# Performance work log

Hardware: AMD Instinct MI355X
Metric: run time of the kernel (lower is better)

The kernel has to match this reference:

```python
import jax, jax.numpy as jnp
import numpy as np
import math

PS = 8  # patch size (hard-coded in module)
DEPTH = 6
LAMBDA_INIT = 0.8 - 0.6 * math.exp(-0.3 * DEPTH)

# torch_dct norm=None DCT-II matrix: y_k = 2 * sum_n x_n cos(pi*(2n+1)k/(2N))
_n = np.arange(PS)
_C = 2.0 * np.cos(np.pi * (2 * _n[None, :] + 1) * _n[:, None] / (2 * PS))  # [k, n]
_Ci = np.linalg.inv(_C)
DCT_M = jnp.asarray(_C, jnp.float32)
IDCT_M = jnp.asarray(_Ci, jnp.float32)


def dct2(x):  # 2D DCT over last two dims (torch_dct.dct_2d, norm=None)
    return jnp.einsum('...mn,am,bn->...ab', x, DCT_M, DCT_M)


def idct2(x):  # exact inverse (torch_dct.idct_2d, norm=None)
    return jnp.einsum('...ab,ma,nb->...mn', x, IDCT_M, IDCT_M)


def conv1x1(x, w):  # w: [O, I]
    return jnp.einsum('oi,bihw->bohw', w, x)


def dw3(x, w):  # depthwise 3x3, stride 1, pad 1; w: [C, 1, 3, 3]
    return jax.lax.conv_general_dilated(
        x, w, window_strides=(1, 1), padding='SAME',
        dimension_numbers=('NCHW', 'OIHW', 'NCHW'),
        feature_group_count=x.shape[1])


def prelu(t, a):
    return jnp.where(t >= 0, t, a * t)


def setup_inputs() -> dict:
    key = jax.random.key(0)
    ks = jax.random.split(key, 20)
    b, c, H, W = 2, 64, 384, 384
    w = lambda k, shape: jax.random.normal(k, shape, jnp.float32) * 0.05
    heads = c // 16
    return {
        'x': jax.random.normal(ks[0], (b, c, H, W), jnp.float32),
        'nir': jax.random.normal(ks[1], (b, c, H, W), jnp.float32),
        'w_hidden': w(ks[2], (c, c)),
        'w_hidden_nir': w(ks[3], (2 * c, c)),
        'w_dw': w(ks[4], (c, 1, 3, 3)),
        'w_dw_nir': w(ks[5], (2 * c, 1, 3, 3)),
        'temperature': jnp.ones((heads, 1, 1), jnp.float32),
        'w_proj_mid': w(ks[6], (c, c)),
        'w_proj_out': w(ks[7], (c, c)),
        'w_p1a': w(ks[8], (c, 1, 3, 3)),
        'a_p1': jnp.asarray(0.25, jnp.float32),
        'w_p1b': w(ks[9], (c, 1, 3, 3)),
        'w_p2a': w(ks[10], (c, 1, 3, 3)),
        'a_p2': jnp.asarray(0.25, jnp.float32),
        'w_p2b': w(ks[11], (c, 1, 3, 3)),
        'lq1': jax.random.normal(ks[12], (c,), jnp.float32) * 0.1,
        'lk1': jax.random.normal(ks[13], (c,), jnp.float32) * 0.1,
        'lq2': jax.random.normal(ks[14], (c,), jnp.float32) * 0.1,
        'lk2': jax.random.normal(ks[15], (c,), jnp.float32) * 0.1,
    }


def reference(x, nir, w_hidden, w_hidden_nir, w_dw, w_dw_nir, temperature,
              w_proj_mid, w_proj_out, w_p1a, a_p1, w_p1b, w_p2a, a_p2, w_p2b,
              lq1, lk1, lq2, lk2):
    b, c, H, W = x.shape
    heads = c // 16
    hh, ww = H // PS, W // PS

    hidden = conv1x1(x, w_hidden)
    nir_hidden = conv1x1(nir, w_hidden_nir)
    q = dw3(hidden, w_dw)
    kv = dw3(nir_hidden, w_dw_nir)
    k, v = kv[:, :c], kv[:, c:]

    # b c (hh p1) (ww p2) -> b c hh ww p1 p2
    patch = lambda t: t.reshape(b, c, hh, PS, ww, PS).transpose(0, 1, 2, 4, 3, 5)
    q_fft = dct2(patch(q))
    k_fft = dct2(patch(k))
    out1 = q_fft * k_fft

    L = hh * ww * PS * PS
    hf = lambda t: t.reshape(b, heads, c // heads, L)  # b head c L
    q_fft, k_fft, out1f = hf(q_fft), hf(k_fft), hf(out1)

    qn = q_fft / jnp.maximum(jnp.linalg.norm(q_fft, axis=-1, keepdims=True), 1e-12)
    kn = k_fft / jnp.maximum(jnp.linalg.norm(k_fft, axis=-1, keepdims=True), 1e-12)

    attn = jax.nn.softmax(jnp.einsum('bhcl,bhdl->bhcd', qn, kn) * temperature, axis=-1)
    o = jnp.einsum('bhcd,bhdl->bhcl', attn, out1f)

    o = o.reshape(b, c, hh, ww, PS, PS)
    o = idct2(o)
    o = o.transpose(0, 1, 2, 4, 3, 5).reshape(b, c, H, W)
    out = conv1x1(o, w_proj_mid)

    lam1 = jnp.exp(jnp.sum(lq1 * lk1))
    lam2 = jnp.exp(jnp.sum(lq2 * lk2))
    lam = lam1 - lam2 + LAMBDA_INIT

    pool = lambda t, wa, a, wb: dw3(prelu(dw3(t, wa), a), wb)
    output = pool(q * out, w_p1a, a_p1, w_p1b) + pool(v - lam * (v * out), w_p2a, a_p2, w_p2b)
    return conv1x1(output, w_proj_out)
```

## Files before the change

kernel.cpp:

```cpp
#include <hip/hip_runtime.h>
#include <cmath>

#ifndef M_PI
#define M_PI 3.14159265358979323846
#endif

#define NB      2
#define N_PIX   147456
#define L_LEN   147456
#define TENS_SZ ((long)NB * 64 * N_PIX)

#define OFF_C    0
#define OFF_CI   64
#define OFF_LAM  128
#define OFF_GRAM 256
#define OFF_QQ   2304
#define OFF_KK   2432
#define OFF_ATTN 2560

#define TW 128
#define TH 16
#define LW 136
#define LH 18
#define PLH 20

__global__ __launch_bounds__(64) void init_k(const float* __restrict__ lq1, const float* __restrict__ lk1,
                                             const float* __restrict__ lq2, const float* __restrict__ lk2,
                                             float* __restrict__ sm) {
  int t = threadIdx.x;
  int a = t >> 3, m = t & 7;
  double cv = 2.0 * cos(M_PI * (double)((2 * m + 1) * a) / 16.0);
  sm[OFF_C + a * 8 + m] = (float)cv;
  sm[OFF_CI + m * 8 + a] = (float)(cv / ((a == 0) ? 32.0 : 16.0));
  float p1 = lq1[t] * lk1[t];
  float p2 = lq2[t] * lk2[t];
  #pragma unroll
  for (int off = 32; off; off >>= 1) {
    p1 += __shfl_xor(p1, off, 64);
    p2 += __shfl_xor(p2, off, 64);
  }
  if (t == 0) sm[OFF_LAM] = expf(p1) - expf(p2) + 0.70082066706704813f;
  for (int i = t; i < 2304; i += 64) sm[OFF_GRAM + i] = 0.f;
}

__global__ void diag_k(float* out, float v) { out[0] = v; }

__global__ __launch_bounds__(256) void conv1x1_k(const float* __restrict__ in, const float* __restrict__ w,
                                                 float* __restrict__ out) {
  __shared__ float ws[4096];
  int t = threadIdx.x;
  for (int j = t; j < 1024; j += 256)
    *reinterpret_cast<float4*>(ws + j * 4) = *reinterpret_cast<const float4*>(w + j * 4);
  __syncthreads();

  long gp = (long)blockIdx.x * 256;
  int bb = (int)(gp / N_PIX);
  int p0 = (int)(gp - (long)bb * N_PIX);
  int lane = t & 63;
  int co0 = (t >> 6) * 16;

  const float* ip = in + (long)bb * 64 * N_PIX + p0 + lane * 4;
  const float* wp = ws + co0 * 64;

  float acc[16][4];
  #pragma unroll
  for (int j = 0; j < 16; j++)
    #pragma unroll
    for (int p = 0; p < 4; p++) acc[j][p] = 0.f;

  for (int c4 = 0; c4 < 16; c4++) {
    float4 x0 = *reinterpret_cast<const float4*>(ip + (long)(c4 * 4 + 0) * N_PIX);
    float4 x1 = *reinterpret_cast<const float4*>(ip + (long)(c4 * 4 + 1) * N_PIX);
    float4 x2 = *reinterpret_cast<const float4*>(ip + (long)(c4 * 4 + 2) * N_PIX);
    float4 x3 = *reinterpret_cast<const float4*>(ip + (long)(c4 * 4 + 3) * N_PIX);
    #pragma unroll
    for (int j = 0; j < 16; j++) {
      float4 w4 = *reinterpret_cast<const float4*>(wp + j * 64 + c4 * 4);
      acc[j][0] = fmaf(w4.x, x0.x, acc[j][0]);
      acc[j][0] = fmaf(w4.y, x1.x, acc[j][0]);
      acc[j][0] = fmaf(w4.z, x2.x, acc[j][0]);
      acc[j][0] = fmaf(w4.w, x3.x, acc[j][0]);
      acc[j][1] = fmaf(w4.x, x0.y, acc[j][1]);
      acc[j][1] = fmaf(w4.y, x1.y, acc[j][1]);
      acc[j][1] = fmaf(w4.z, x2.y, acc[j][1]);
      acc[j][1] = fmaf(w4.w, x3.y, acc[j][1]);
      acc[j][2] = fmaf(w4.x, x0.z, acc[j][2]);
      acc[j][2] = fmaf(w4.y, x1.z, acc[j][2]);
      acc[j][2] = fmaf(w4.z, x2.z, acc[j][2]);
      acc[j][2] = fmaf(w4.w, x3.z, acc[j][2]);
      acc[j][3] = fmaf(w4.x, x0.w, acc[j][3]);
      acc[j][3] = fmaf(w4.y, x1.w, acc[j][3]);
      acc[j][3] = fmaf(w4.z, x2.w, acc[j][3]);
      acc[j][3] = fmaf(w4.w, x3.w, acc[j][3]);
    }
  }

  float* op = out + (long)bb * 64 * N_PIX + p0 + lane * 4;
  #pragma unroll
  for (int j = 0; j < 16; j++)
    *reinterpret_cast<float4*>(op + (long)(co0 + j) * N_PIX) =
        make_float4(acc[j][0], acc[j][1], acc[j][2], acc[j][3]);
}

__global__ __launch_bounds__(256) void conv1x1_nir2_k(const float* __restrict__ in, const float* __restrict__ w,
                                                      float* __restrict__ outk, float* __restrict__ outv) {
  __shared__ float ws[4096];
  int t = threadIdx.x;
  long gp = (long)blockIdx.x * 256;
  int bb = (int)(gp / N_PIX);
  int p0 = (int)(gp - (long)bb * N_PIX);
  int lane = t & 63;
  int co0 = (t >> 6) * 16;
  const float* ip = in + (long)bb * 64 * N_PIX + p0 + lane * 4;

  for (int half = 0; half < 2; half++) {
    __syncthreads();
    for (int j = t; j < 1024; j += 256)
      *reinterpret_cast<float4*>(ws + j * 4) = *reinterpret_cast<const float4*>(w + half * 4096 + j * 4);
    __syncthreads();
    const float* wp = ws + co0 * 64;
    float acc[16][4];
    #pragma unroll
    for (int j = 0; j < 16; j++)
      #pragma unroll
      for (int p = 0; p < 4; p++) acc[j][p] = 0.f;
    for (int c4 = 0; c4 < 16; c4++) {
      float4 x0 = *reinterpret_cast<const float4*>(ip + (long)(c4 * 4 + 0) * N_PIX);
      float4 x1 = *reinterpret_cast<const float4*>(ip + (long)(c4 * 4 + 1) * N_PIX);
      float4 x2 = *reinterpret_cast<const float4*>(ip + (long)(c4 * 4 + 2) * N_PIX);
      float4 x3 = *reinterpret_cast<const float4*>(ip + (long)(c4 * 4 + 3) * N_PIX);
      #pragma unroll
      for (int j = 0; j < 16; j++) {
        float4 w4 = *reinterpret_cast<const float4*>(wp + j * 64 + c4 * 4);
        acc[j][0] = fmaf(w4.x, x0.x, acc[j][0]);
        acc[j][0] = fmaf(w4.y, x1.x, acc[j][0]);
        acc[j][0] = fmaf(w4.z, x2.x, acc[j][0]);
        acc[j][0] = fmaf(w4.w, x3.x, acc[j][0]);
        acc[j][1] = fmaf(w4.x, x0.y, acc[j][1]);
        acc[j][1] = fmaf(w4.y, x1.y, acc[j][1]);
        acc[j][1] = fmaf(w4.z, x2.y, acc[j][1]);
        acc[j][1] = fmaf(w4.w, x3.y, acc[j][1]);
        acc[j][2] = fmaf(w4.x, x0.z, acc[j][2]);
        acc[j][2] = fmaf(w4.y, x1.z, acc[j][2]);
        acc[j][2] = fmaf(w4.z, x2.z, acc[j][2]);
        acc[j][2] = fmaf(w4.w, x3.z, acc[j][2]);
        acc[j][3] = fmaf(w4.x, x0.w, acc[j][3]);
        acc[j][3] = fmaf(w4.y, x1.w, acc[j][3]);
        acc[j][3] = fmaf(w4.z, x2.w, acc[j][3]);
        acc[j][3] = fmaf(w4.w, x3.w, acc[j][3]);
      }
    }
    float* op = (half ? outv : outk) + (long)bb * 64 * N_PIX + p0 + lane * 4;
    #pragma unroll
    for (int j = 0; j < 16; j++)
      *reinterpret_cast<float4*>(op + (long)(co0 + j) * N_PIX) =
          make_float4(acc[j][0], acc[j][1], acc[j][2], acc[j][3]);
  }
}

__device__ __forceinline__ float4 load_g4(const float* __restrict__ p, int gy, int gx) {
  if ((unsigned)gy >= 384u) return make_float4(0.f, 0.f, 0.f, 0.f);
  if (gx >= 0 && gx + 3 < 384) return *reinterpret_cast<const float4*>(p + gy * 384 + gx);
  float e[4];
  #pragma unroll
  for (int i = 0; i < 4; i++) {
    int xx = gx + i;
    e[i] = ((unsigned)xx < 384u) ? p[gy * 384 + xx] : 0.f;
  }
  return make_float4(e[0], e[1], e[2], e[3]);
}

__global__ __launch_bounds__(256) void dw3t_k(const float* __restrict__ in, const float* __restrict__ w,
                                              float* __restrict__ out) {
  __shared__ float sT[LH * LW];
  int plane = blockIdx.z;
  int ch = plane & 63;
  int x0 = blockIdx.x * TW, y0 = blockIdx.y * TH;
  const float* ip = in + (long)plane * N_PIX;
  int t = threadIdx.x;
  for (int j = t; j < LH * 34; j += 256) {
    int row = j / 34, c4 = j - row * 34;
    *reinterpret_cast<float4*>(sT + row * LW + c4 * 4) = load_g4(ip, y0 - 1 + row, x0 - 4 + c4 * 4);
  }
  __syncthreads();
  const float* wp = w + ch * 9;
  float w00 = wp[0], w01 = wp[1], w02 = wp[2];
  float w10 = wp[3], w11 = wp[4], w12 = wp[5];
  float w20 = wp[6], w21 = wp[7], w22 = wp[8];
  int col = t & 127, rg = t >> 7;
  int lc = col + 4;
  int r0 = rg * 8;
  float a0 = sT[r0 * LW + lc - 1],       a1 = sT[r0 * LW + lc],       a2 = sT[r0 * LW + lc + 1];
  float b0 = sT[(r0 + 1) * LW + lc - 1], b1 = sT[(r0 + 1) * LW + lc], b2 = sT[(r0 + 1) * LW + lc + 1];
  float* op = out + (long)plane * N_PIX + (long)(y0 + rg * 8) * 384 + x0 + col;
  #pragma unroll
  for (int i = 0; i < 8; i++) {
    int lr = r0 + i + 2;
    float c0 = sT[lr * LW + lc - 1], c1 = sT[lr * LW + lc], c2 = sT[lr * LW + lc + 1];
    float s = w00 * a0;
    s = fmaf(w01, a1, s); s = fmaf(w02, a2, s);
    s = fmaf(w10, b0, s); s = fmaf(w11, b1, s); s = fmaf(w12, b2, s);
    s = fmaf(w20, c0, s); s = fmaf(w21, c1, s); s = fmaf(w22, c2, s);
    op[i * 384] = s;
    a0 = b0; a1 = b1; a2 = b2;
    b0 = c0; b1 = c1; b2 = c2;
  }
}

__global__ __launch_bounds__(256) void dw3dct_k(const float* __restrict__ in, const float* __restrict__ w,
                                                const float* __restrict__ sm,
                                                float* __restrict__ outf, float* __restrict__ outs) {
  __shared__ float sT[LH * LW];
  __shared__ float Cm[64];
  int t = threadIdx.x;
  if (t < 64) Cm[t] = sm[OFF_C + t];
  int plane = blockIdx.z;
  int ch = plane & 63;
  int x0 = blockIdx.x * TW, y0 = blockIdx.y * TH;
  const float* ip = in + (long)plane * N_PIX;
  for (int j = t; j < LH * 34; j += 256) {
    int row = j / 34, c4 = j - row * 34;
    *reinterpret_cast<float4*>(sT + row * LW + c4 * 4) = load_g4(ip, y0 - 1 + row, x0 - 4 + c4 * 4);
  }
  __syncthreads();
  const float* wp = w + ch * 9;
  float w00 = wp[0], w01 = wp[1], w02 = wp[2];
  float w10 = wp[3], w11 = wp[4], w12 = wp[5];
  float w20 = wp[6], w21 = wp[7], w22 = wp[8];
  int col = t & 127, rg = t >> 7;
  int lc = col + 4;
  int r0 = rg * 8;
  float r[8];
  {
    float a0 = sT[r0 * LW + lc - 1],       a1 = sT[r0 * LW + lc],       a2 = sT[r0 * LW + lc + 1];
    float b0 = sT[(r0 + 1) * LW + lc - 1], b1 = sT[(r0 + 1) * LW + lc], b2 = sT[(r0 + 1) * LW + lc + 1];
    #pragma unroll
    for (int i = 0; i < 8; i++) {
      int lr = r0 + i + 2;
      float c0 = sT[lr * LW + lc - 1], c1 = sT[lr * LW + lc], c2 = sT[lr * LW + lc + 1];
      float s = w00 * a0;
      s = fmaf(w01, a1, s); s = fmaf(w02, a2, s);
      s = fmaf(w10, b0, s); s = fmaf(w11, b1, s); s = fmaf(w12, b2, s);
      s = fmaf(w20, c0, s); s = fmaf(w21, c1, s); s = fmaf(w22, c2, s);
      r[i] = s;
      a0 = b0; a1 = b1; a2 = b2;
      b0 = c0; b1 = c1; b2 = c2;
    }
  }
  if (outs) {
    float* op = outs + (long)plane * N_PIX + (long)(y0 + r0) * 384 + x0 + col;
    #pragma unroll
    for (int i = 0; i < 8; i++) op[i * 384] = r[i];
  }
  __syncthreads();
  #pragma unroll
  for (int i = 0; i < 8; i++) sT[(r0 + i + 1) * LW + lc] = r[i];
  __syncthreads();
  int patch = t >> 3, a = t & 7;
  int prow = patch >> 4, pcol = patch & 15;
  const float* xb = sT + (prow * 8 + 1) * LW + pcol * 8 + 4;
  float T[8];
  #pragma unroll
  for (int n = 0; n < 8; n++) {
    float s = 0.f;
    #pragma unroll
    for (int m = 0; m < 8; m++) s = fmaf(Cm[a * 8 + m], xb[m * LW + n], s);
    T[n] = s;
  }
  float o[8];
  #pragma unroll
  for (int b8 = 0; b8 < 8; b8++) {
    float s = 0.f;
    #pragma unroll
    for (int n = 0; n < 8; n++) s = fmaf(Cm[b8 * 8 + n], T[n], s);
    o[b8] = s;
  }
  int py = (y0 >> 3) + prow, px = (x0 >> 3) + pcol;
  float* op = outf + (long)plane * L_LEN + (long)(py * 48 + px) * 64 + a * 8;
  *reinterpret_cast<float4*>(op)     = make_float4(o[0], o[1], o[2], o[3]);
  *reinterpret_cast<float4*>(op + 4) = make_float4(o[4], o[5], o[6], o[7]);
}

__device__ __forceinline__ void stencil_col9(const float* __restrict__ sb, int ci, int rs0,
                                             float w00, float w01, float w02,
                                             float w10, float w11, float w12,
                                             float w20, float w21, float w22,
                                             float alpha, bool xok, int y0,
                                             float* __restrict__ r) {
  float a0 = sb[rs0 * LW + ci - 1],       a1 = sb[rs0 * LW + ci],       a2 = sb[rs0 * LW + ci + 1];
  float b0 = sb[(rs0 + 1) * LW + ci - 1], b1 = sb[(rs0 + 1) * LW + ci], b2 = sb[(rs0 + 1) * LW + ci + 1];
  #pragma unroll
  for (int ii = 0; ii < 9; ii++) {
    int rs2 = rs0 + ii + 2;
    float c0 = sb[rs2 * LW + ci - 1], c1 = sb[rs2 * LW + ci], c2 = sb[rs2 * LW + ci + 1];
    float s = w00 * a0;
    s = fmaf(w01, a1, s); s = fmaf(w02, a2, s);
    s = fmaf(w10, b0, s); s = fmaf(w11, b1, s); s = fmaf(w12, b2, s);
    s = fmaf(w20, c0, s); s = fmaf(w21, c1, s); s = fmaf(w22, c2, s);
    s = (s >= 0.f) ? s : alpha * s;
    int gy = y0 - 1 + rs0 + ii;
    r[ii] = (xok && (unsigned)gy < 384u) ? s : 0.f;
    a0 = b0; a1 = b1; a2 = b2;
    b0 = c0; b1 = c1; b2 = c2;
  }
}

__global__ __launch_bounds__(256) void pool_k(const float* __restrict__ q, const float* __restrict__ om,
                                              const float* __restrict__ v,
                                              const float* __restrict__ w1a, const float* __restrict__ a1p,
                                              const float* __restrict__ w1b,
                                              const float* __restrict__ w2a, const float* __restrict__ a2p,
                                              const float* __restrict__ w2b,
                                              const float* __restrict__ sm,
                                              float* __restrict__ outp) {
  __shared__ float s1[PLH * LW], s2[PLH * LW];
  int plane = blockIdx.z;
  int ch = plane & 63;
  int x0 = blockIdx.x * TW, y0 = blockIdx.y * TH;
  const float* qp = q  + (long)plane * N_PIX;
  const float* op = om + (long)plane * N_PIX;
  const float* vp = v  + (long)plane * N_PIX;
  float lam = sm[OFF_LAM];
  int t = threadIdx.x;
  for (int j = t; j < PLH * 34; j += 256) {
    int row = j / 34, c4 = j - row * 34;
    int gy = y0 - 2 + row, gx = x0 - 4 + c4 * 4;
    float4 qv = load_g4(qp, gy, gx);
    float4 ov = load_g4(op, gy, gx);
    float4 vv = load_g4(vp, gy, gx);
    *reinterpret_cast<float4*>(s1 + row * LW + c4 * 4) =
        make_float4(qv.x * ov.x, qv.y * ov.y, qv.z * ov.z, qv.w * ov.w);
    *reinterpret_cast<float4*>(s2 + row * LW + c4 * 4) =
        make_float4(vv.x - lam * vv.x * ov.x, vv.y - lam * vv.y * ov.y,
                    vv.z - lam * vv.z * ov.z, vv.w - lam * vv.w * ov.w);
  }
  __syncthreads();

  int ct = t & 127, rg = t >> 7;
  int rs0 = rg * 9;
  int ci0 = 3 + ct;
  int ci1 = 131 + ct;
  bool xok0 = (unsigned)(x0 - 4 + ci0) < 384u;
  bool xok1 = (unsigned)(x0 - 4 + ci1) < 384u;

  {
    const float* wp1 = w1a + ch * 9;
    float w00 = wp1[0], w01 = wp1[1], w02 = wp1[2], w10 = wp1[3], w11 = wp1[4],
          w12 = wp1[5], w20 = wp1[6], w21 = wp1[7], w22 = wp1[8];
    float alpha = a1p[0];
    float rm[9], re[9];
    stencil_col9(s1, ci0, rs0, w00, w01, w02, w10, w11, w12, w20, w21, w22, alpha, xok0, y0, rm);
    if (ct < 2)
      stencil_col9(s1, ci1, rs0, w00, w01, w02, w10, w11, w12, w20, w21, w22, alpha, xok1, y0, re);
    __syncthreads();
    #pragma unroll
    for (int ii = 0; ii < 9; ii++) s1[(rs0 + ii + 1) * LW + ci0] = rm[ii];
    if (ct < 2) {
      #pragma unroll
      for (int ii = 0; ii < 9; ii++) s1[(rs0 + ii + 1) * LW + ci1] = re[ii];
    }
  }
  {
    const float* wp2 = w2a + ch * 9;
    float w00 = wp2[0], w01 = wp2[1], w02 = wp2[2], w10 = wp2[3], w11 = wp2[4],
          w12 = wp2[5], w20 = wp2[6], w21 = wp2[7], w22 = wp2[8];
    float alpha = a2p[0];
    float rm[9], re[9];
    stencil_col9(s2, ci0, rs0, w00, w01, w02, w10, w11, w12, w20, w21, w22, alpha, xok0, y0, rm);
    if (ct < 2)
      stencil_col9(s2, ci1, rs0, w00, w01, w02, w10, w11, w12, w20, w21, w22, alpha, xok1, y0, re);
    __syncthreads();
    #pragma unroll
    for (int ii = 0; ii < 9; ii++) s2[(rs0 + ii + 1) * LW + ci0] = rm[ii];
    if (ct < 2) {
      #pragma unroll
      for (int ii = 0; ii < 9; ii++) s2[(rs0 + ii + 1) * LW + ci1] = re[ii];
    }
  }
  __syncthreads();
  {
    const float* wp1 = w1b + ch * 9;
    const float* wp2 = w2b + ch * 9;
    float p00 = wp1[0], p01 = wp1[1], p02 = wp1[2], p10 = wp1[3], p11 = wp1[4], p12 = wp1[5], p20 = wp1[6], p21 = wp1[7], p22 = wp1[8];
    float q00 = wp2[0], q01 = wp2[1], q02 = wp2[2], q10 = wp2[3], q11 = wp2[4], q12 = wp2[5], q20 = wp2[6], q21 = wp2[7], q22 = wp2[8];
    int col = t & 127, rg2 = t >> 7;
    int lc = col + 4;
    int rb = rg2 * 8 + 1;
    float xa0 = s1[rb * LW + lc - 1],       xa1 = s1[rb * LW + lc],       xa2 = s1[rb * LW + lc + 1];
    float xb0 = s1[(rb + 1) * LW + lc - 1], xb1 = s1[(rb + 1) * LW + lc], xb2 = s1[(rb + 1) * LW + lc + 1];
    float ya0 = s2[rb * LW + lc - 1],       ya1 = s2[rb * LW + lc],       ya2 = s2[rb * LW + lc + 1];
    float yb0 = s2[(rb + 1) * LW + lc - 1], yb1 = s2[(rb + 1) * LW + lc], yb2 = s2[(rb + 1) * LW + lc + 1];
    float* wo = outp + (long)plane * N_PIX + (long)(y0 + rg2 * 8) * 384 + x0 + col;
    #pragma unroll
    for (int i = 0; i < 8; i++) {
      int lr = rb + i + 2;
      float xc0 = s1[lr * LW + lc - 1], xc1 = s1[lr * LW + lc], xc2 = s1[lr * LW + lc + 1];
      float yc0 = s2[lr * LW + lc - 1], yc1 = s2[lr * LW + lc], yc2 = s2[lr * LW + lc + 1];
      float s = p00 * xa0;
      s = fmaf(p01, xa1, s); s = fmaf(p02, xa2, s);
      s = fmaf(p10, xb0, s); s = fmaf(p11, xb1, s); s = fmaf(p12, xb2, s);
      s = fmaf(p20, xc0, s); s = fmaf(p21, xc1, s); s = fmaf(p22, xc2, s);
      s = fmaf(q00, ya0, s); s = fmaf(q01, ya1, s); s = fmaf(q02, ya2, s);
      s = fmaf(q10, yb0, s); s = fmaf(q11, yb1, s); s = fmaf(q12, yb2, s);
      s = fmaf(q20, yc0, s); s = fmaf(q21, yc1, s); s = fmaf(q22, yc2, s);
      wo[i * 384] = s;
      xa0 = xb0; xa1 = xb1; xa2 = xb2; xb0 = xc0; xb1 = xc1; xb2 = xc2;
      ya0 = yb0; ya1 = yb1; ya2 = yb2; yb0 = yc0; yb1 = yc1; yb2 = yc2;
    }
  }
}

__global__ __launch_bounds__(256) void dct_k(const float* __restrict__ in,
                                             const float* __restrict__ sm, float* __restrict__ outf) {
  __shared__ float Cm[64];
  if (threadIdx.x < 64) Cm[threadIdx.x] = sm[OFF_C + threadIdx.x];
  __syncthreads();
  int pid = blockIdx.x * 256 + threadIdx.x;
  int wx = pid % 48;
  int t1 = pid / 48;
  int hy = t1 % 48; t1 /= 48;
  int ch = t1 & 63;
  int bb = t1 >> 6;
  const float* ip = in + (long)(bb * 64 + ch) * N_PIX + (hy * 8) * 384 + wx * 8;
  float X[8][8];
  #pragma unroll
  for (int r = 0; r < 8; r++) {
    float4 v0 = *reinterpret_cast<const float4*>(ip + r * 384);
    float4 v1 = *reinterpret_cast<const float4*>(ip + r * 384 + 4);
    X[r][0] = v0.x; X[r][1] = v0.y; X[r][2] = v0.z; X[r][3] = v0.w;
    X[r][4] = v1.x; X[r][5] = v1.y; X[r][6] = v1.z; X[r][7] = v1.w;
  }
  float T[8][8];
  #pragma unroll
  for (int a = 0; a < 8; a++)
    #pragma unroll
    for (int n = 0; n < 8; n++) {
      float s = 0.f;
      #pragma unroll
      for (int m = 0; m < 8; m++) s = fmaf(Cm[a * 8 + m], X[m][n], s);
      T[a][n] = s;
    }
  #pragma unroll
  for (int a = 0; a < 8; a++)
    #pragma unroll
    for (int b8 = 0; b8 < 8; b8++) {
      float s = 0.f;
      #pragma unroll
      for (int n = 0; n < 8; n++) s = fmaf(Cm[b8 * 8 + n], T[a][n], s);
      X[a][b8] = s;
    }
  float* op = outf + (long)(bb * 64 + ch) * L_LEN + (long)(hy * 48 + wx) * 64;
  float4* o4 = reinterpret_cast<float4*>(op);
  #pragma unroll
  for (int a = 0; a < 8; a++) {
    o4[a * 2]     = make_float4(X[a][0], X[a][1], X[a][2], X[a][3]);
    o4[a * 2 + 1] = make_float4(X[a][4], X[a][5], X[a][6], X[a][7]);
  }
}

#define GS_P 132
__global__ __launch_bounds__(256) void gram_k(const float* __restrict__ qf, const float* __restrict__ kf,
                                              float* __restrict__ sm) {
  __shared__ float qs[16 * GS_P], ks[16 * GS_P];
  int t = threadIdx.x;
  int bh = blockIdx.y;
  int bb = bh >> 2, h = bh & 3;
  const float* qbase = qf + ((long)bb * 64 + h * 16) * L_LEN;
  const float* kbase = kf + ((long)bb * 64 + h * 16) * L_LEN;
  int c = t >> 4, d = t & 15;
  long l0 = (long)blockIdx.x * 2048;
  float g = 0.f, nq = 0.f, nk = 0.f;
  for (int chunk = 0; chunk < 16; chunk++) {
    long lc = l0 + chunk * 128;
    __syncthreads();
    for (int j = t; j < 512; j += 256) {
      int row = j >> 5, c4 = j & 31;
      *reinterpret_cast<float4*>(qs + row * GS_P + c4 * 4) =
          *reinterpret_cast<const float4*>(qbase + (long)row * L_LEN + lc + c4 * 4);
      *reinterpret_cast<float4*>(ks + row * GS_P + c4 * 4) =
          *reinterpret_cast<const float4*>(kbase + (long)row * L_LEN + lc + c4 * 4);
    }
    __syncthreads();
    #pragma unroll
    for (int i = 0; i < 128; i += 4) {
      float4 a = *reinterpret_cast<const float4*>(qs + c * GS_P + i);
      float4 b = *reinterpret_cast<const float4*>(ks + d * GS_P + i);
      g  = fmaf(a.x, b.x, g);  g  = fmaf(a.y, b.y, g);  g  = fmaf(a.z, b.z, g);  g  = fmaf(a.w, b.w, g);
      nq = fmaf(a.x, a.x, nq); nq = fmaf(a.y, a.y, nq); nq = fmaf(a.z, a.z, nq); nq = fmaf(a.w, a.w, nq);
      nk = fmaf(b.x, b.x, nk); nk = fmaf(b.y, b.y, nk); nk = fmaf(b.z, b.z, nk); nk = fmaf(b.w, b.w, nk);
    }
  }
  atomicAdd(&sm[OFF_GRAM + bh * 256 + c * 16 + d], g);
  if (d == 0) atomicAdd(&sm[OFF_QQ + bh * 16 + c], nq);
  if (c == 0) atomicAdd(&sm[OFF_KK + bh * 16 + d], nk);
}

__global__ __launch_bounds__(256) void attn_k(const float* __restrict__ temp, float* __restrict__ sm) {
  int bh = blockIdx.x;
  int h = bh & 3;
  int t = threadIdx.x;
  int c = t >> 4, d = t & 15;
  float qn = fmaxf(sqrtf(sm[OFF_QQ + bh * 16 + c]), 1e-12f);
  float kn = fmaxf(sqrtf(sm[OFF_KK + bh * 16 + d]), 1e-12f);
  float v = sm[OFF_GRAM + bh * 256 + t] / (qn * kn) * temp[h];
  float mx = v;
  #pragma unroll
  for (int o = 8; o; o >>= 1) mx = fmaxf(mx, __shfl_xor(mx, o, 16));
  float e = expf(v - mx);
  float s = e;
  #pragma unroll
  for (int o = 8; o; o >>= 1) s += __shfl_xor(s, o, 16);
  sm[OFF_ATTN + bh * 256 + t] = e / s;
}

#define CB_P 273
__global__ __launch_bounds__(256) void comb_idct_k(const float* __restrict__ qf, const float* __restrict__ kf,
                                                   const float* __restrict__ sm, float* __restrict__ out) {
  __shared__ float A[256];
  __shared__ float Ci[64];
  __shared__ float sb[16 * CB_P];
  int bh = blockIdx.y;
  int t = threadIdx.x;
  A[t] = sm[OFF_ATTN + bh * 256 + t];
  if (t < 64) Ci[t] = sm[OFF_CI + t];
  __syncthreads();
  int bb = bh >> 2, h = bh & 3;
  long l = (long)blockIdx.x * 256 + t;
  const float* qp = qf + ((long)bb * 64 + h * 16) * L_LEN + l;
  const float* kp = kf + ((long)bb * 64 + h * 16) * L_LEN + l;
  float p[16];
  #pragma unroll
  for (int d = 0; d < 16; d++) p[d] = qp[(long)d * L_LEN] * kp[(long)d * L_LEN];
  int pl_w = t >> 6, i_w = t & 63;
  #pragma unroll
  for (int c = 0; c < 16; c++) {
    float s = 0.f;
    #pragma unroll
    for (int d = 0; d < 16; d++) s = fmaf(A[c * 16 + d], p[d], s);
    sb[c * CB_P + pl_w * 68 + i_w] = s;
  }
  __syncthreads();
  int j = t & 3, c = (t >> 2) & 15, pl = t >> 6;
  const float* fb = sb + c * CB_P + pl * 68;
  float F[8][8];
  #pragma unroll
  for (int a = 0; a < 8; a++)
    #pragma unroll
    for (int b8 = 0; b8 < 8; b8++) F[a][b8] = fb[a * 8 + b8];
  int patch = blockIdx.x * 4 + pl;
  int hy = patch / 48, wx = patch - hy * 48;
  float* op = out + ((long)bb * 64 + h * 16 + c) * N_PIX + (long)(hy * 8) * 384 + wx * 8;
  #pragma unroll
  for (int mm = 0; mm < 2; mm++) {
    int m = 2 * j + mm;
    float T[8];
    #pragma unroll
    for (int b8 = 0; b8 < 8; b8++) {
      float s = 0.f;
      #pragma unroll
      for (int a = 0; a < 8; a++) s = fmaf(Ci[m * 8 + a], F[a][b8], s);
      T[b8] = s;
    }
    float o[8];
    #pragma unroll
    for (int n = 0; n < 8; n++) {
      float s = 0.f;
      #pragma unroll
      for (int b8 = 0; b8 < 8; b8++) s = fmaf(Ci[n * 8 + b8], T[b8], s);
      o[n] = s;
    }
    *reinterpret_cast<float4*>(op + m * 384)     = make_float4(o[0], o[1], o[2], o[3]);
    *reinterpret_cast<float4*>(op + m * 384 + 4) = make_float4(o[4], o[5], o[6], o[7]);
  }
}

__global__ __launch_bounds__(256) void combine_k(float* __restrict__ qf, const float* __restrict__ kf,
                                                 const float* __restrict__ sm) {
  __shared__ float A[256];
  int bh = blockIdx.y;
  A[threadIdx.x] = sm[OFF_ATTN + bh * 256 + threadIdx.x];
  __syncthreads();
  int bb = bh >> 2, h = bh & 3;
  long l = (long)blockIdx.x * 256 + threadIdx.x;
  float* qp = qf + ((long)bb * 64 + h * 16) * L_LEN + l;
  const float* kp = kf + ((long)bb * 64 + h * 16) * L_LEN + l;
  float p[16];
  #pragma unroll
  for (int d = 0; d < 16; d++) p[d] = qp[(long)d * L_LEN] * kp[(long)d * L_LEN];
  #pragma unroll
  for (int c = 0; c < 16; c++) {
    float s = 0.f;
    #pragma unroll
    for (int d = 0; d < 16; d++) s = fmaf(A[c * 16 + d], p[d], s);
    qp[(long)c * L_LEN] = s;
  }
}

__global__ __launch_bounds__(256) void idct_k(const float* __restrict__ inf, const float* __restrict__ sm,
                                              float* __restrict__ out) {
  __shared__ float Ci[64];
  if (threadIdx.x < 64) Ci[threadIdx.x] = sm[OFF_CI + threadIdx.x];
  __syncthreads();
  int pid = blockIdx.x * 256 + threadIdx.x;
  int wx = pid % 48;
  int t1 = pid / 48;
  int hy = t1 % 48; t1 /= 48;
  int ch = t1 & 63;
  int bb = t1 >> 6;
  const float4* i4 = reinterpret_cast<const float4*>(inf + (long)(bb * 64 + ch) * L_LEN + (long)(hy * 48 + wx) * 64);
  float F[8][8];
  #pragma unroll
  for (int a = 0; a < 8; a++) {
    float4 v0 = i4[a * 2], v1 = i4[a * 2 + 1];
    F[a][0] = v0.x; F[a][1] = v0.y; F[a][2] = v0.z; F[a][3] = v0.w;
    F[a][4] = v1.x; F[a][5] = v1.y; F[a][6] = v1.z; F[a][7] = v1.w;
  }
  float T[8][8];
  #pragma unroll
  for (int m = 0; m < 8; m++)
    #pragma unroll
    for (int b8 = 0; b8 < 8; b8++) {
      float s = 0.f;
      #pragma unroll
      for (int a = 0; a < 8; a++) s = fmaf(Ci[m * 8 + a], F[a][b8], s);
      T[m][b8] = s;
    }
  #pragma unroll
  for (int m = 0; m < 8; m++)
    #pragma unroll
    for (int n = 0; n < 8; n++) {
      float s = 0.f;
      #pragma unroll
      for (int b8 = 0; b8 < 8; b8++) s = fmaf(Ci[n * 8 + b8], T[m][b8], s);
      F[m][n] = s;
    }
  float* op = out + (long)(bb * 64 + ch) * N_PIX + (hy * 8) * 384 + wx * 8;
  #pragma unroll
  for (int m = 0; m < 8; m++) {
    *reinterpret_cast<float4*>(op + m * 384)     = make_float4(F[m][0], F[m][1], F[m][2], F[m][3]);
    *reinterpret_cast<float4*>(op + m * 384 + 4) = make_float4(F[m][4], F[m][5], F[m][6], F[m][7]);
  }
}

extern "C" void kernel_launch(void* const* d_in, const int* in_sizes, int n_in,
                              void* d_out, int out_size, void* d_ws, size_t ws_size,
                              hipStream_t stream) {
  const float* x            = (const float*)d_in[0];
  const float* nir          = (const float*)d_in[1];
  const float* w_hidden     = (const float*)d_in[2];
  const float* w_hidden_nir = (const float*)d_in[3];
  const float* w_dw         = (const float*)d_in[4];
  const float* w_dw_nir     = (const float*)d_in[5];
  const float* temperature  = (const float*)d_in[6];
  const float* w_proj_mid   = (const float*)d_in[7];
  const float* w_proj_out   = (const float*)d_in[8];
  const float* w_p1a        = (const float*)d_in[9];
  const float* a_p1         = (const float*)d_in[10];
  const float* w_p1b        = (const float*)d_in[11];
  const float* w_p2a        = (const float*)d_in[12];
  const float* a_p2         = (const float*)d_in[13];
  const float* w_p2b        = (const float*)d_in[14];
  const float* lq1          = (const float*)d_in[15];
  const float* lk1          = (const float*)d_in[16];
  const float* lq2          = (const float*)d_in[17];
  const float* lk2          = (const float*)d_in[18];

  float* OUT = (float*)d_out;
  float* W0 = (float*)d_ws;
  float* W1 = W0 + TENS_SZ;
  float* W2 = W1 + TENS_SZ;
  float* SM = W2 + TENS_SZ;
  float* W3 = SM + 8192;

  size_t needed3 = (size_t)3 * TENS_SZ * sizeof(float) + 32768;
  size_t needed4 = ((size_t)4 * TENS_SZ + 8192) * sizeof(float);
  if (ws_size < needed3) {
    diag_k<<<1, 1, 0, stream>>>(OUT, 1000.0f + (float)(ws_size >> 20));
    return;
  }
  bool big = ws_size >= needed4;

  dim3 blk256(256);
  dim3 gridST(3, 24, NB * 64);

  init_k<<<1, 64, 0, stream>>>(lq1, lk1, lq2, lk2, SM);

  if (big) {
    conv1x1_nir2_k<<<1152, blk256, 0, stream>>>(nir, w_hidden_nir, W0, W1);
    dw3t_k<<<gridST, blk256, 0, stream>>>(W1, w_dw_nir + 64 * 9, W2);
    dw3dct_k<<<gridST, blk256, 0, stream>>>(W0, w_dw_nir, SM, W1, nullptr);
    conv1x1_k<<<1152, blk256, 0, stream>>>(x, w_hidden, W0);
    dw3dct_k<<<gridST, blk256, 0, stream>>>(W0, w_dw, SM, W3, OUT);
    gram_k<<<dim3(72, 8), blk256, 0, stream>>>(W3, W1, SM);
    attn_k<<<8, blk256, 0, stream>>>(temperature, SM);
    comb_idct_k<<<dim3(576, 8), blk256, 0, stream>>>(W3, W1, SM, W0);
    conv1x1_k<<<1152, blk256, 0, stream>>>(W0, w_proj_mid, W1);
    pool_k<<<gridST, blk256, 0, stream>>>(OUT, W1, W2, w_p1a, a_p1, w_p1b, w_p2a, a_p2, w_p2b, SM, W3);
    conv1x1_k<<<1152, blk256, 0, stream>>>(W3, w_proj_out, OUT);
  } else {
    conv1x1_k<<<1152, blk256, 0, stream>>>(x, w_hidden, W0);
    dw3t_k<<<gridST, blk256, 0, stream>>>(W0, w_dw, OUT);
    conv1x1_k<<<1152, blk256, 0, stream>>>(nir, w_hidden_nir, W0);
    dw3t_k<<<gridST, blk256, 0, stream>>>(W0, w_dw_nir, W1);
    conv1x1_k<<<1152, blk256, 0, stream>>>(nir, w_hidden_nir + 64 * 64, W0);
    dw3t_k<<<gridST, blk256, 0, stream>>>(W0, w_dw_nir + 64 * 9, W2);
    dct_k<<<1152, blk256, 0, stream>>>(W1, SM, W0);
    dct_k<<<1152, blk256, 0, stream>>>(OUT, SM, W1);
    gram_k<<<dim3(72, 8), blk256, 0, stream>>>(W1, W0, SM);
    attn_k<<<8, blk256, 0, stream>>>(temperature, SM);
    combine_k<<<dim3(576, 8), blk256, 0, stream>>>(W1, W0, SM);
    idct_k<<<1152, blk256, 0, stream>>>(W1, SM, W0);
    conv1x1_k<<<1152, blk256, 0, stream>>>(W0, w_proj_mid, W1);
    pool_k<<<gridST, blk256, 0, stream>>>(OUT, W1, W2, w_p1a, a_p1, w_p1b, w_p2a, a_p2, w_p2b, SM, W0);
    conv1x1_k<<<1152, blk256, 0, stream>>>(W0, w_proj_out, OUT);
  }
}
```

Before: 751.2 us.

## Fuse the v depthwise conv into the pool kernel, removing a separate pass

The depthwise 3x3 conv that produces v from the nir hidden features now runs inside a new pool2_k kernel instead of a standalone dw3t_k launch. pool2_k loads the pre-conv v tile with a wider halo, computes v in shared memory, applies the lambda modulation, and then runs the two pooling stencil chains. Workspace buffers are renumbered to fit. This removes one full-tensor write and read plus one kernel launch. In exchange it adds halo recomputation, extra shared memory and extra syncs in the pool kernel.

```diff
diff --git a/kernel.cpp b/kernel.cpp
--- a/kernel.cpp
+++ b/kernel.cpp
@@ -23,6 +23,7 @@
 #define LW 136
 #define LH 18
 #define PLH 20
+#define PVH 22
 
 __global__ __launch_bounds__(64) void init_k(const float* __restrict__ lq1, const float* __restrict__ lk1,
                                              const float* __restrict__ lq2, const float* __restrict__ lk2,
@@ -305,6 +306,27 @@
   }
 }
 
+__device__ __forceinline__ void dw3_col10(const float* __restrict__ sb, int ci, int rs0,
+                                          float w00, float w01, float w02,
+                                          float w10, float w11, float w12,
+                                          float w20, float w21, float w22,
+                                          float* __restrict__ r) {
+  float a0 = sb[rs0 * LW + ci - 1],       a1 = sb[rs0 * LW + ci],       a2 = sb[rs0 * LW + ci + 1];
+  float b0 = sb[(rs0 + 1) * LW + ci - 1], b1 = sb[(rs0 + 1) * LW + ci], b2 = sb[(rs0 + 1) * LW + ci + 1];
+  #pragma unroll
+  for (int ii = 0; ii < 10; ii++) {
+    int rs2 = rs0 + ii + 2;
+    float c0 = sb[rs2 * LW + ci - 1], c1 = sb[rs2 * LW + ci], c2 = sb[rs2 * LW + ci + 1];
+    float s = w00 * a0;
+    s = fmaf(w01, a1, s); s = fmaf(w02, a2, s);
+    s = fmaf(w10, b0, s); s = fmaf(w11, b1, s); s = fmaf(w12, b2, s);
+    s = fmaf(w20, c0, s); s = fmaf(w21, c1, s); s = fmaf(w22, c2, s);
+    r[ii] = s;
+    a0 = b0; a1 = b1; a2 = b2;
+    b0 = c0; b1 = c1; b2 = c2;
+  }
+}
+
 __global__ __launch_bounds__(256) void pool_k(const float* __restrict__ q, const float* __restrict__ om,
                                               const float* __restrict__ v,
                                               const float* __restrict__ w1a, const float* __restrict__ a1p,
@@ -396,6 +418,153 @@
       int lr = rb + i + 2;
       float xc0 = s1[lr * LW + lc - 1], xc1 = s1[lr * LW + lc], xc2 = s1[lr * LW + lc + 1];
       float yc0 = s2[lr * LW + lc - 1], yc1 = s2[lr * LW + lc], yc2 = s2[lr * LW + lc + 1];
+      float s = p00 * xa0;
+      s = fmaf(p01, xa1, s); s = fmaf(p02, xa2, s);
+      s = fmaf(p10, xb0, s); s = fmaf(p11, xb1, s); s = fmaf(p12, xb2, s);
+      s = fmaf(p20, xc0, s); s = fmaf(p21, xc1, s); s = fmaf(p22, xc2, s);
+      s = fmaf(q00, ya0, s); s = fmaf(q01, ya1, s); s = fmaf(q02, ya2, s);
+      s = fmaf(q10, yb0, s); s = fmaf(q11, yb1, s); s = fmaf(q12, yb2, s);
+      s = fmaf(q20, yc0, s); s = fmaf(q21, yc1, s); s = fmaf(q22, yc2, s);
+      wo[i * 384] = s;
+      xa0 = xb0; xa1 = xb1; xa2 = xb2; xb0 = xc0; xb1 = xc1; xb2 = xc2;
+      ya0 = yb0; ya1 = yb1; ya2 = yb2; yb0 = yc0; yb1 = yc1; yb2 = yc2;
+    }
+  }
+}
+
+__global__ __launch_bounds__(256) void pool2_k(const float* __restrict__ q, const float* __restrict__ om,
+                                               const float* __restrict__ vpre,
+                                               const float* __restrict__ wv,
+                                               const float* __restrict__ w1a, const float* __restrict__ a1p,
+                                               const float* __restrict__ w1b,
+                                               const float* __restrict__ w2a, const float* __restrict__ a2p,
+                                               const float* __restrict__ w2b,
+                                               const float* __restrict__ sm,
+                                               float* __restrict__ outp) {
+  __shared__ float s1[PLH * LW];
+  __shared__ float s2[PVH * LW];
+  int plane = blockIdx.z;
+  int ch = plane & 63;
+  int x0 = blockIdx.x * TW, y0 = blockIdx.y * TH;
+  const float* qp = q + (long)plane * N_PIX;
+  const float* omp_ = om + (long)plane * N_PIX;
+  const float* vp = vpre + (long)plane * N_PIX;
+  float lam = sm[OFF_LAM];
+  int t = threadIdx.x;
+  for (int j = t; j < PVH * 34; j += 256) {
+    int row = j / 34, c4 = j - row * 34;
+    *reinterpret_cast<float4*>(s2 + row * LW + c4 * 4) = load_g4(vp, y0 - 3 + row, x0 - 4 + c4 * 4);
+  }
+  for (int j = t; j < PLH * 34; j += 256) {
+    int row = j / 34, c4 = j - row * 34;
+    int gy = y0 - 2 + row, gx = x0 - 4 + c4 * 4;
+    float4 qv = load_g4(qp, gy, gx);
+    float4 ov = load_g4(omp_, gy, gx);
+    *reinterpret_cast<float4*>(s1 + row * LW + c4 * 4) =
+        make_float4(qv.x * ov.x, qv.y * ov.y, qv.z * ov.z, qv.w * ov.w);
+  }
+  __syncthreads();
+
+  int ct = t & 127, rg = t >> 7;
+  float p2m[10], p2e[10];
+  int rsV = rg * 10;
+  int ciV0 = 2 + ct;
+  int ciV1 = 130 + ct;
+  {
+    const float* wp = wv + ch * 9;
+    float w00 = wp[0], w01 = wp[1], w02 = wp[2], w10 = wp[3], w11 = wp[4],
+          w12 = wp[5], w20 = wp[6], w21 = wp[7], w22 = wp[8];
+    dw3_col10(s2, ciV0, rsV, w00, w01, w02, w10, w11, w12, w20, w21, w22, p2m);
+    if (ct < 4)
+      dw3_col10(s2, ciV1, rsV, w00, w01, w02, w10, w11, w12, w20, w21, w22, p2e);
+    int gx0 = x0 - 4 + ciV0, gx1 = x0 - 4 + ciV1;
+    bool vx0 = (unsigned)gx0 < 384u, vx1 = (unsigned)gx1 < 384u;
+    #pragma unroll
+    for (int ii = 0; ii < 10; ii++) {
+      int gy = y0 - 2 + rsV + ii;
+      bool oky = (unsigned)gy < 384u;
+      if (oky && vx0) {
+        float o = omp_[gy * 384 + gx0];
+        float vv = p2m[ii];
+        p2m[ii] = vv - lam * vv * o;
+      } else p2m[ii] = 0.f;
+      if (ct < 4) {
+        if (oky && vx1) {
+          float o = omp_[gy * 384 + gx1];
+          float vv = p2e[ii];
+          p2e[ii] = vv - lam * vv * o;
+        } else p2e[ii] = 0.f;
+      }
+    }
+  }
+  __syncthreads();
+  #pragma unroll
+  for (int ii = 0; ii < 10; ii++) s2[(rsV + 1 + ii) * LW + ciV0] = p2m[ii];
+  if (ct < 4) {
+    #pragma unroll
+    for (int ii = 0; ii < 10; ii++) s2[(rsV + 1 + ii) * LW + ciV1] = p2e[ii];
+  }
+  int rs0 = rg * 9;
+  int ci0 = 3 + ct, ci1 = 131 + ct;
+  bool xok0 = (unsigned)(x0 - 4 + ci0) < 384u;
+  bool xok1 = (unsigned)(x0 - 4 + ci1) < 384u;
+  float u1m[9], u1e[9];
+  {
+    const float* wp1 = w1a + ch * 9;
+    float w00 = wp1[0], w01 = wp1[1], w02 = wp1[2], w10 = wp1[3], w11 = wp1[4],
+          w12 = wp1[5], w20 = wp1[6], w21 = wp1[7], w22 = wp1[8];
+    float alpha = a1p[0];
+    stencil_col9(s1, ci0, rs0, w00, w01, w02, w10, w11, w12, w20, w21, w22, alpha, xok0, y0, u1m);
+    if (ct < 2)
+      stencil_col9(s1, ci1, rs0, w00, w01, w02, w10, w11, w12, w20, w21, w22, alpha, xok1, y0, u1e);
+  }
+  __syncthreads();
+  #pragma unroll
+  for (int ii = 0; ii < 9; ii++) s1[(rs0 + ii + 1) * LW + ci0] = u1m[ii];
+  if (ct < 2) {
+    #pragma unroll
+    for (int ii = 0; ii < 9; ii++) s1[(rs0 + ii + 1) * LW + ci1] = u1e[ii];
+  }
+  float u2m[9], u2e[9];
+  {
+    const float* wp2 = w2a + ch * 9;
+    float w00 = wp2[0], w01 = wp2[1], w02 = wp2[2], w10 = wp2[3], w11 = wp2[4],
+          w12 = wp2[5], w20 = wp2[6], w21 = wp2[7], w22 = wp2[8];
+    float alpha = a2p[0];
+    stencil_col9(s2 + LW, ci0, rs0, w00, w01, w02, w10, w11, w12, w20, w21, w22, alpha, xok0, y0, u2m);
+    if (ct < 2)
+      stencil_col9(s2 + LW, ci1, rs0, w00, w01, w02, w10, w11, w12, w20, w21, w22, alpha, xok1, y0, u2e);
+  }
+  __syncthreads();
+  {
+    float* s2u = s2 + LW;
+    #pragma unroll
+    for (int ii = 0; ii < 9; ii++) s2u[(rs0 + ii + 1) * LW + ci0] = u2m[ii];
+    if (ct < 2) {
+      #pragma unroll
+      for (int ii = 0; ii < 9; ii++) s2u[(rs0 + ii + 1) * LW + ci1] = u2e[ii];
+    }
+  }
+  __syncthreads();
+  {
+    const float* s2u = s2 + LW;
+    const float* wp1 = w1b + ch * 9;
+    const float* wp2 = w2b + ch * 9;
+    float p00 = wp1[0], p01 = wp1[1], p02 = wp1[2], p10 = wp1[3], p11 = wp1[4], p12 = wp1[5], p20 = wp1[6], p21 = wp1[7], p22 = wp1[8];
+    float q00 = wp2[0], q01 = wp2[1], q02 = wp2[2], q10 = wp2[3], q11 = wp2[4], q12 = wp2[5], q20 = wp2[6], q21 = wp2[7], q22 = wp2[8];
+    int col = t & 127, rg2 = t >> 7;
+    int lc = col + 4;
+    int rb = rg2 * 8 + 1;
+    float xa0 = s1[rb * LW + lc - 1],        xa1 = s1[rb * LW + lc],        xa2 = s1[rb * LW + lc + 1];
+    float xb0 = s1[(rb + 1) * LW + lc - 1],  xb1 = s1[(rb + 1) * LW + lc],  xb2 = s1[(rb + 1) * LW + lc + 1];
+    float ya0 = s2u[rb * LW + lc - 1],       ya1 = s2u[rb * LW + lc],       ya2 = s2u[rb * LW + lc + 1];
+    float yb0 = s2u[(rb + 1) * LW + lc - 1], yb1 = s2u[(rb + 1) * LW + lc], yb2 = s2u[(rb + 1) * LW + lc + 1];
+    float* wo = outp + (long)plane * N_PIX + (long)(y0 + rg2 * 8) * 384 + x0 + col;
+    #pragma unroll
+    for (int i = 0; i < 8; i++) {
+      int lr = rb + i + 2;
+      float xc0 = s1[lr * LW + lc - 1],  xc1 = s1[lr * LW + lc],  xc2 = s1[lr * LW + lc + 1];
+      float yc0 = s2u[lr * LW + lc - 1], yc1 = s2u[lr * LW + lc], yc2 = s2u[lr * LW + lc + 1];
       float s = p00 * xa0;
       s = fmaf(p01, xa1, s); s = fmaf(p02, xa2, s);
       s = fmaf(p10, xb0, s); s = fmaf(p11, xb1, s); s = fmaf(p12, xb2, s);
@@ -687,15 +856,15 @@
 
   if (big) {
     conv1x1_nir2_k<<<1152, blk256, 0, stream>>>(nir, w_hidden_nir, W0, W1);
-    dw3t_k<<<gridST, blk256, 0, stream>>>(W1, w_dw_nir + 64 * 9, W2);
-    dw3dct_k<<<gridST, blk256, 0, stream>>>(W0, w_dw_nir, SM, W1, nullptr);
+    dw3dct_k<<<gridST, blk256, 0, stream>>>(W0, w_dw_nir, SM, W2, nullptr);
     conv1x1_k<<<1152, blk256, 0, stream>>>(x, w_hidden, W0);
     dw3dct_k<<<gridST, blk256, 0, stream>>>(W0, w_dw, SM, W3, OUT);
-    gram_k<<<dim3(72, 8), blk256, 0, stream>>>(W3, W1, SM);
+    gram_k<<<dim3(72, 8), blk256, 0, stream>>>(W3, W2, SM);
     attn_k<<<8, blk256, 0, stream>>>(temperature, SM);
-    comb_idct_k<<<dim3(576, 8), blk256, 0, stream>>>(W3, W1, SM, W0);
-    conv1x1_k<<<1152, blk256, 0, stream>>>(W0, w_proj_mid, W1);
-    pool_k<<<gridST, blk256, 0, stream>>>(OUT, W1, W2, w_p1a, a_p1, w_p1b, w_p2a, a_p2, w_p2b, SM, W3);
+    comb_idct_k<<<dim3(576, 8), blk256, 0, stream>>>(W3, W2, SM, W0);
+    conv1x1_k<<<1152, blk256, 0, stream>>>(W0, w_proj_mid, W2);
+    pool2_k<<<gridST, blk256, 0, stream>>>(OUT, W2, W1, w_dw_nir + 64 * 9,
+                                           w_p1a, a_p1, w_p1b, w_p2a, a_p2, w_p2b, SM, W3);
     conv1x1_k<<<1152, blk256, 0, stream>>>(W3, w_proj_out, OUT);
   } else {
     conv1x1_k<<<1152, blk256, 0, stream>>>(x, w_hidden, W0);
```

Measured after the change: 763.1 us. Within noise of the previous version (+1.6%).
